# Kernel tuning notes

Hardware: AMD Instinct MI355X
Metric: run time of the kernel (lower is better)

## Reference

```python
import jax, jax.numpy as jnp
import numpy as np

ENC_HID = 512
DEC_HID = 1024
ATTN_DIM = 1024
ATTN_IN = ENC_HID * 2 + DEC_HID  # 2048
B, S = 32, 1024


def setup_inputs() -> dict:
    key = jax.random.key(0)
    k1, k2, k3, k4, k5 = jax.random.split(key, 5)
    decoder_hidden = jax.random.normal(k1, (B, DEC_HID), dtype=jnp.float32)
    encoder_outputs = jax.random.normal(k2, (B, S, 2 * ENC_HID), dtype=jnp.float32)
    # nn.Linear(attn_in, attn_dim): weight [attn_dim, attn_in], bias [attn_dim]
    lim = 1.0 / np.sqrt(ATTN_IN)
    W = jax.random.uniform(k3, (ATTN_IN, ATTN_DIM), jnp.float32, -lim, lim)
    b = jax.random.uniform(k4, (ATTN_DIM,), jnp.float32, -lim, lim)
    v = jax.random.uniform(k5, (ATTN_DIM,), jnp.float32, 0.0, 1.0)
    return {"decoder_hidden": decoder_hidden, "encoder_outputs": encoder_outputs,
            "W": W, "b": b, "v": v}


def reference(decoder_hidden, encoder_outputs, W, b, v):
    # Avoid materializing the repeat+concat: split the Linear weight into the
    # decoder-hidden block and the encoder-outputs block. Same math as
    # tanh(Linear(cat([dec_rep, enc], -1))).
    W_dec = W[:DEC_HID]          # [dec_hid, attn_dim]
    W_enc = W[DEC_HID:]          # [2*enc_hid, attn_dim]
    dec_proj = decoder_hidden @ W_dec + b                     # [B, A]
    enc_proj = jnp.einsum('bse,ea->bsa', encoder_outputs, W_enc)  # [B, S, A]
    energy = jnp.tanh(enc_proj + dec_proj[:, None, :])        # [B, S, A]
    attention = jnp.einsum('bsa,a->bs', energy, v)            # [B, S]
    return jax.nn.softmax(attention, axis=1)
```

## Files before the change

### kernel.cpp

```cpp
#include <hip/hip_runtime.h>
#include <stdint.h>

#define ENC2 1024
#define DECH 1024
#define ADIM 1024
#define BB   32
#define SS   1024

typedef _Float16 half_t;
typedef __attribute__((ext_vector_type(4))) _Float16 half4;
typedef __attribute__((ext_vector_type(8))) _Float16 half8;
typedef __attribute__((ext_vector_type(4))) float    f32x4;

__device__ __forceinline__ void dma16(const half_t* g, half_t* l) {
    __builtin_amdgcn_global_load_lds((const __attribute__((address_space(1))) void*)g,
                                     (__attribute__((address_space(3))) void*)l,
                                     16, 0, 0);
}

#define VM6()   asm volatile("s_waitcnt vmcnt(6)" ::: "memory")
#define VM3()   asm volatile("s_waitcnt vmcnt(3)" ::: "memory")
#define VM0()   asm volatile("s_waitcnt vmcnt(0)" ::: "memory")
#define LGKM0() asm volatile("s_waitcnt lgkmcnt(0)" ::: "memory")
#define SCHED0() __builtin_amdgcn_sched_barrier(0)
#define RBAR()  __builtin_amdgcn_s_barrier()

__global__ __launch_bounds__(512) void k_prep(const float* __restrict__ enc,
                                              const float* __restrict__ W,
                                              const float* __restrict__ dh,
                                              half_t* __restrict__ e16,
                                              half_t* __restrict__ Wt2,
                                              float* __restrict__ dpart) {
    __shared__ __align__(16) char smem[33792];
    const int bid = blockIdx.x;
    const int t = threadIdx.x;

    if (bid < 2048) {
        half_t (*Lt)[264] = (half_t (*)[264])smem;
        const int rblk = bid >> 2, cblk = bid & 3;
        const int r0 = rblk * 64, k0 = cblk * 256;
        #pragma unroll
        for (int i = 0; i < 8; i++) {
            int row = i * 8 + (t >> 6);
            int col = (t & 63) * 4;
            float4 vv = *(const float4*)&enc[(size_t)(r0 + row) * ENC2 + k0 + col];
            half4 h;
            h[0] = (half_t)vv.x; h[1] = (half_t)vv.y;
            h[2] = (half_t)vv.z; h[3] = (half_t)vv.w;
            *(half4*)&Lt[row][col] = h;
        }
        __syncthreads();
        const int mi = rblk >> 1, p = rblk & 1;
        const int ks0 = cblk * 8;
        #pragma unroll
        for (int j = 0; j < 4; j++) {
            int u = j * 512 + t;
            int pair = u >> 6, l = u & 63;
            int ksl = pair >> 2, quad = pair & 3;
            half8 h = *(const half8*)&Lt[l][ksl * 32 + quad * 8];
            size_t chunk = (size_t)(mi * 32 + ks0 + ksl) * 8 + quad * 2 + p;
            *(half8*)&e16[(chunk << 9) + l * 8] = h;
        }
    } else if (bid < 2176) {
        float (*tile)[257] = (float (*)[257])smem;
        const int blk = bid - 2048;
        const int nb = blk >> 5;
        const int ks = blk & 31;
        #pragma unroll
        for (int i = 0; i < 16; i++) {
            int idx = t + i * 512;
            int kr = idx >> 8, n = idx & 255;
            tile[kr][n] = W[(size_t)(DECH + ks * 32 + kr) * ADIM + nb * 256 + n];
        }
        __syncthreads();
        half_t* reg = Wt2 + ((size_t)(nb * 32 + ks) << 13);
        #pragma unroll
        for (int i = 0; i < 2; i++) {
            int cid = t + i * 512;
            int r = cid >> 2, pos = cid & 3;
            int c = pos ^ ((r >> 1) & 3);
            half8 h;
            #pragma unroll
            for (int e = 0; e < 8; e++) h[e] = (half_t)tile[c * 8 + e][r];
            *(half8*)(reg + r * 32 + pos * 8) = h;
        }
    } else {
        float (*red)[BB][64] = (float (*)[BB][64])smem;
        const int blk = bid - 2176;
        const int ct = blk & 15;
        const int kc = blk >> 4;
        if (t < 256) {
            const int col = ct * 64 + (t & 63);
            const int w = t >> 6;
            const int k0 = kc * 128 + w * 32;
            float wreg[32];
            #pragma unroll
            for (int kk = 0; kk < 32; kk++)
                wreg[kk] = W[(size_t)(k0 + kk) * ADIM + col];
            float s[BB];
            #pragma unroll
            for (int b = 0; b < BB; b++) s[b] = 0.f;
            #pragma unroll
            for (int kk = 0; kk < 32; kk++) {
                #pragma unroll
                for (int b = 0; b < BB; b++)
                    s[b] += dh[b * DECH + k0 + kk] * wreg[kk];
            }
            #pragma unroll
            for (int b = 0; b < BB; b++) red[w][b][t & 63] = s[b];
        }
        __syncthreads();
        if (t < 64) {
            for (int b = 0; b < BB; b++)
                dpart[((size_t)kc * BB + b) * ADIM + ct * 64 + t] =
                    red[0][b][t] + red[1][b][t] + red[2][b][t] + red[3][b][t];
        }
    }
}

#define BM 128
#define BN 256
#define BK 32

__global__ __launch_bounds__(512, 4) void k_main(const half_t* __restrict__ encA,
                                                 const half_t* __restrict__ Wt2,
                                                 const float* __restrict__ dpart,
                                                 const float* __restrict__ bias,
                                                 const float* __restrict__ v,
                                                 float* __restrict__ scores_part) {
    __shared__ half_t lsA[3][4096];
    __shared__ half_t lsB[3][8192];

    const int bid = blockIdx.x;
    const int mi = (bid >> 5) * 8 + (bid & 7);
    const int nb = (bid >> 3) & 3;
    const int m0 = mi * BM;
    const int t = threadIdx.x;
    const int w = t >> 6, L = t & 63;
    const int wm = w & 1, wn = w >> 1;
    const int lane15 = L & 15, quad = L >> 4;

    const half_t* Abase = encA + ((size_t)mi << 17);
    const half_t* Bbase = Wt2 + ((size_t)(nb * 32) << 13);

    f32x4 acc[4][4];
    #pragma unroll
    for (int i = 0; i < 4; i++)
        #pragma unroll
        for (int j = 0; j < 4; j++) acc[i][j] = (f32x4)0.f;

    auto stage = [&](int ks, int pb) {
        dma16(Abase + (((size_t)ks * 8 + w) << 9) + L * 8, &lsA[pb][w * 512]);
        #pragma unroll
        for (int jj = 0; jj < 2; jj++) {
            int j = 2 * w + jj;
            dma16(Bbase + ((size_t)ks << 13) + j * 512 + L * 8,
                  &lsB[pb][j * 512]);
        }
    };

    stage(0, 0);
    stage(1, 1);

    int cur = 0;
    for (int ks = 0; ks < ENC2 / BK; ks++) {
        const int nxt = (cur == 0) ? 2 : cur - 1;
        if (ks < ENC2 / BK - 2) {
            stage(ks + 2, nxt);
            VM6();
        } else if (ks == ENC2 / BK - 2) {
            VM3();
        } else {
            VM0();
        }
        RBAR();
        SCHED0();

        half8 af[4], bf[4];
        #pragma unroll
        for (int sm = 0; sm < 4; sm++)
            af[sm] = *(const half8*)&lsA[cur][quad * 1024 +
                                              (wm * 64 + sm * 16 + lane15) * 8];
        #pragma unroll
        for (int sn = 0; sn < 4; sn++) {
            int r = wn * 64 + sn * 16 + lane15;
            int pos = quad ^ ((r >> 1) & 3);
            bf[sn] = *(const half8*)&lsB[cur][r * 32 + pos * 8];
        }
        LGKM0();
        SCHED0();
        #pragma unroll
        for (int sm = 0; sm < 4; sm++)
            #pragma unroll
            for (int sn = 0; sn < 4; sn++)
                acc[sm][sn] = __builtin_amdgcn_mfma_f32_16x16x32_f16(
                    af[sm], bf[sn], acc[sm][sn], 0, 0, 0);
        RBAR();
        cur = (cur == 2) ? 0 : cur + 1;
    }

    const int batch = mi >> 3;
    float vv[4], dp[4];
    #pragma unroll
    for (int sn = 0; sn < 4; sn++) {
        int ng = nb * BN + wn * 64 + sn * 16 + lane15;
        vv[sn] = v[ng];
        float s = bias[ng];
        #pragma unroll
        for (int kc = 0; kc < 8; kc++)
            s += dpart[((size_t)kc * BB + batch) * ADIM + ng];
        dp[sn] = s;
    }

    float* redL = (float*)&lsA[0][0];
    #pragma unroll
    for (int sm = 0; sm < 4; sm++) {
        #pragma unroll
        for (int rr = 0; rr < 4; rr++) {
            float s = 0.f;
            #pragma unroll
            for (int sn = 0; sn < 4; sn++) {
                float x = acc[sm][sn][rr] + dp[sn];
                float e  = __builtin_amdgcn_exp2f(x * 2.8853900817779268f);
                float th = 1.f - 2.f * __builtin_amdgcn_rcpf(e + 1.f);
                s += th * vv[sn];
            }
            s += __shfl_xor(s, 1, 64);
            s += __shfl_xor(s, 2, 64);
            s += __shfl_xor(s, 4, 64);
            s += __shfl_xor(s, 8, 64);
            if (lane15 == 0) {
                int mlocal = wm * 64 + sm * 16 + quad * 4 + rr;
                redL[wn * 128 + mlocal] = s;
            }
        }
    }
    __syncthreads();
    if (t < 128) {
        float s = redL[t] + redL[128 + t] + redL[256 + t] + redL[384 + t];
        scores_part[((size_t)nb << 15) + m0 + t] = s;
    }
}

__global__ __launch_bounds__(256) void k_softmax(const float* __restrict__ sp,
                                                 float* __restrict__ out) {
    __shared__ float red[8];
    const int b = blockIdx.x, t = threadIdx.x;
    float x[4];
    #pragma unroll
    for (int i = 0; i < 4; i++) {
        size_t idx = (size_t)b * SS + t + i * 256;
        x[i] = sp[idx] + sp[(1u << 15) + idx] + sp[(2u << 15) + idx] +
               sp[(3u << 15) + idx];
    }
    float mx = fmaxf(fmaxf(x[0], x[1]), fmaxf(x[2], x[3]));
    #pragma unroll
    for (int d = 1; d < 64; d <<= 1) mx = fmaxf(mx, __shfl_xor(mx, d, 64));
    if ((t & 63) == 0) red[t >> 6] = mx;
    __syncthreads();
    mx = fmaxf(fmaxf(red[0], red[1]), fmaxf(red[2], red[3]));
    float e[4], s = 0.f;
    #pragma unroll
    for (int i = 0; i < 4; i++) {
        e[i] = __builtin_amdgcn_exp2f((x[i] - mx) * 1.4426950408889634f);
        s += e[i];
    }
    #pragma unroll
    for (int d = 1; d < 64; d <<= 1) s += __shfl_xor(s, d, 64);
    if ((t & 63) == 0) red[4 + (t >> 6)] = s;
    __syncthreads();
    s = red[4] + red[5] + red[6] + red[7];
    float inv = 1.f / s;
    #pragma unroll
    for (int i = 0; i < 4; i++) out[(size_t)b * SS + t + i * 256] = e[i] * inv;
}

__global__ __launch_bounds__(256) void k_wt_f(const float* __restrict__ W,
                                              half_t* __restrict__ Wt2) {
    __shared__ float tile[32][257];
    const int nb = blockIdx.x >> 5;
    const int ks = blockIdx.x & 31;
    const int t = threadIdx.x;
    #pragma unroll
    for (int i = 0; i < 32; i++) {
        int idx = t + i * 256;
        int kr = idx >> 8, n = idx & 255;
        tile[kr][n] = W[(size_t)(DECH + ks * 32 + kr) * ADIM + nb * 256 + n];
    }
    __syncthreads();
    half_t* reg = Wt2 + ((size_t)(nb * 32 + ks) << 13);
    #pragma unroll
    for (int i = 0; i < 4; i++) {
        int cid = t + i * 256;
        int r = cid >> 2, pos = cid & 3;
        int c = pos ^ ((r >> 1) & 3);
        half8 h;
        #pragma unroll
        for (int e = 0; e < 8; e++) h[e] = (half_t)tile[c * 8 + e][r];
        *(half8*)(reg + r * 32 + pos * 8) = h;
    }
}

__global__ __launch_bounds__(256) void k_dp1_f(const float* __restrict__ dh,
                                               const float* __restrict__ W,
                                               float* __restrict__ part) {
    __shared__ float red[4][BB][64];
    const int t = threadIdx.x;
    const int ct = blockIdx.x & 15;
    const int kc = blockIdx.x >> 4;
    const int col = ct * 64 + (t & 63);
    const int w = t >> 6;
    const int k0 = kc * 128 + w * 32;
    float wreg[32];
    #pragma unroll
    for (int kk = 0; kk < 32; kk++)
        wreg[kk] = W[(size_t)(k0 + kk) * ADIM + col];
    float s[BB];
    #pragma unroll
    for (int b = 0; b < BB; b++) s[b] = 0.f;
    #pragma unroll
    for (int kk = 0; kk < 32; kk++) {
        #pragma unroll
        for (int b = 0; b < BB; b++)
            s[b] += dh[b * DECH + k0 + kk] * wreg[kk];
    }
    #pragma unroll
    for (int b = 0; b < BB; b++) red[w][b][t & 63] = s[b];
    __syncthreads();
    if (t < 64) {
        for (int b = 0; b < BB; b++)
            part[((size_t)kc * BB + b) * ADIM + ct * 64 + t] =
                red[0][b][t] + red[1][b][t] + red[2][b][t] + red[3][b][t];
    }
}

__global__ __launch_bounds__(256) void k_dp2_f(const float* __restrict__ part,
                                               const float* __restrict__ bias,
                                               float* __restrict__ decp) {
    const int i = blockIdx.x * 256 + threadIdx.x;
    float s = bias[i & (ADIM - 1)];
    #pragma unroll
    for (int kc = 0; kc < 8; kc++)
        s += part[(size_t)kc * BB * ADIM + i];
    decp[i] = s;
}

#define LDA 40
__global__ __launch_bounds__(512, 4) void k_main_reg(const float* __restrict__ enc,
                                                     const half_t* __restrict__ Wt2,
                                                     const float* __restrict__ decp,
                                                     const float* __restrict__ v,
                                                     float* __restrict__ scores_part) {
    __shared__ half_t lsA[2][BM][LDA];
    __shared__ half_t lsB[2][BN * BK];

    const int bid = blockIdx.x;
    const int mi = (bid >> 5) * 8 + (bid & 7);
    const int nb = (bid >> 3) & 3;
    const int m0 = mi * BM;
    const int t = threadIdx.x;
    const int w = t >> 6, L = t & 63;
    const int wm = w & 1, wn = w >> 1;
    const int lane15 = L & 15, quad = L >> 4;

    const int arow = t & 127;
    const int akc  = (t >> 7) * 8;
    const float* Aptr = enc + (size_t)(m0 + arow) * ENC2 + akc;
    const half_t* Bbase = Wt2 + ((size_t)(nb * 32) << 13);

    f32x4 acc[4][4];
    #pragma unroll
    for (int i = 0; i < 4; i++)
        #pragma unroll
        for (int j = 0; j < 4; j++) acc[i][j] = (f32x4)0.f;

    float4 ra0, ra1;
    auto loadA = [&](int ks) {
        const float* p = Aptr + ks * BK;
        ra0 = *(const float4*)p;
        ra1 = *(const float4*)(p + 4);
    };
    auto writeA = [&](int pb) {
        half8 ha;
        ha[0] = (half_t)ra0.x; ha[1] = (half_t)ra0.y;
        ha[2] = (half_t)ra0.z; ha[3] = (half_t)ra0.w;
        ha[4] = (half_t)ra1.x; ha[5] = (half_t)ra1.y;
        ha[6] = (half_t)ra1.z; ha[7] = (half_t)ra1.w;
        *(half8*)&lsA[pb][arow][akc] = ha;
    };
    auto dmaB = [&](int ks, int pb) {
        #pragma unroll
        for (int jj = 0; jj < 2; jj++) {
            int j = 2 * w + jj;
            dma16(Bbase + ((size_t)ks << 13) + j * 512 + L * 8,
                  &lsB[pb][j * 512]);
        }
    };

    dmaB(0, 0);
    loadA(0);
    writeA(0);
    loadA(1);
    __syncthreads();

    for (int ks = 0; ks < ENC2 / BK; ks++) {
        const int cur = ks & 1;
        if (ks < ENC2 / BK - 1) {
            dmaB(ks + 1, cur ^ 1);
            writeA(cur ^ 1);
            if (ks < ENC2 / BK - 2) loadA(ks + 2);
        }
        half8 af[4], bf[4];
        #pragma unroll
        for (int sm = 0; sm < 4; sm++)
            af[sm] = *(const half8*)&lsA[cur][wm * 64 + sm * 16 + lane15][quad * 8];
        #pragma unroll
        for (int sn = 0; sn < 4; sn++) {
            int r = wn * 64 + sn * 16 + lane15;
            int pos = quad ^ ((r >> 1) & 3);
            bf[sn] = *(const half8*)&lsB[cur][r * 32 + pos * 8];
        }
        #pragma unroll
        for (int sm = 0; sm < 4; sm++)
            #pragma unroll
            for (int sn = 0; sn < 4; sn++)
                acc[sm][sn] = __builtin_amdgcn_mfma_f32_16x16x32_f16(
                    af[sm], bf[sn], acc[sm][sn], 0, 0, 0);
        __syncthreads();
    }

    const int batch = mi >> 3;
    float vv[4], dp[4];
    #pragma unroll
    for (int sn = 0; sn < 4; sn++) {
        int ng = nb * BN + wn * 64 + sn * 16 + lane15;
        vv[sn] = v[ng];
        dp[sn] = decp[(size_t)batch * ADIM + ng];
    }

    float* redL = (float*)&lsA[0][0][0];
    #pragma unroll
    for (int sm = 0; sm < 4; sm++) {
        #pragma unroll
        for (int rr = 0; rr < 4; rr++) {
            float s = 0.f;
            #pragma unroll
            for (int sn = 0; sn < 4; sn++) {
                float x = acc[sm][sn][rr] + dp[sn];
                float e  = __builtin_amdgcn_exp2f(x * 2.8853900817779268f);
                float th = 1.f - 2.f * __builtin_amdgcn_rcpf(e + 1.f);
                s += th * vv[sn];
            }
            s += __shfl_xor(s, 1, 64);
            s += __shfl_xor(s, 2, 64);
            s += __shfl_xor(s, 4, 64);
            s += __shfl_xor(s, 8, 64);
            if (lane15 == 0) {
                int mlocal = wm * 64 + sm * 16 + quad * 4 + rr;
                redL[wn * 128 + mlocal] = s;
            }
        }
    }
    __syncthreads();
    if (t < 128) {
        float s = redL[t] + redL[128 + t] + redL[256 + t] + redL[384 + t];
        scores_part[((size_t)nb << 15) + m0 + t] = s;
    }
}

extern "C" void kernel_launch(void* const* d_in, const int* in_sizes, int n_in,
                              void* d_out, int out_size, void* d_ws, size_t ws_size,
                              hipStream_t stream) {
    const float* dh   = (const float*)d_in[0];
    const float* enc  = (const float*)d_in[1];
    const float* W    = (const float*)d_in[2];
    const float* bias = (const float*)d_in[3];
    const float* v    = (const float*)d_in[4];
    float* out = (float*)d_out;

    char* ws = (char*)d_ws;
    const size_t E16_BYTES = (size_t)BB * SS * ENC2 * sizeof(half_t);
    const size_t NEED = (4u << 20) + E16_BYTES;

    if (ws_size >= NEED) {
        half_t* Wt2   = (half_t*)ws;
        float*  dpart = (float*)(ws + (2u << 20));
        float*  spart = (float*)(ws + (3u << 20));
        half_t* e16   = (half_t*)(ws + (4u << 20));

        k_prep   <<<2304, 512, 0, stream>>>(enc, W, dh, e16, Wt2, dpart);
        k_main   <<<1024, 512, 0, stream>>>(e16, Wt2, dpart, bias, v, spart);
        k_softmax<<<32, 256, 0, stream>>>(spart, out);
    } else {
        half_t* Wt2   = (half_t*)ws;
        float*  decp  = (float*)(ws + 2u * 1024 * 1024);
        float*  spart = (float*)(ws + 2u * 1024 * 1024 + 128 * 1024);
        float*  dpart = (float*)(ws + 2u * 1024 * 1024 + 640 * 1024);

        k_wt_f   <<<128, 256, 0, stream>>>(W, Wt2);
        k_dp1_f  <<<128, 256, 0, stream>>>(dh, W, dpart);
        k_dp2_f  <<<128, 256, 0, stream>>>(dpart, bias, decp);
        k_main_reg<<<1024, 512, 0, stream>>>(enc, Wt2, decp, v, spart);
        k_softmax<<<32, 256, 0, stream>>>(spart, out);
    }
}
```

Before: 281.3 us.

## Store fp16 encoder in row-major order and gather tiles directly in GEMM DMA

The prep kernel no longer reorders the fp16 encoder copy into a tiled chunk layout through shared memory. It now does a straight elementwise fp32-to-fp16 conversion in row-major order. The GEMM's global-to-LDS DMA addresses are changed to pull each lane's 16-byte piece from the row-major matrix at stride 1024. This drops the LDS transpose and its barrier from the prep pass, but the GEMM's A loads become strided per lane instead of contiguous 1 KB chunks, which may reduce coalescing.

```diff
diff --git a/kernel.cpp b/kernel.cpp
--- a/kernel.cpp
+++ b/kernel.cpp
@@ -36,30 +36,18 @@
     const int t = threadIdx.x;
 
     if (bid < 2048) {
-        half_t (*Lt)[264] = (half_t (*)[264])smem;
-        const int rblk = bid >> 2, cblk = bid & 3;
-        const int r0 = rblk * 64, k0 = cblk * 256;
-        #pragma unroll
-        for (int i = 0; i < 8; i++) {
-            int row = i * 8 + (t >> 6);
-            int col = (t & 63) * 4;
-            float4 vv = *(const float4*)&enc[(size_t)(r0 + row) * ENC2 + k0 + col];
-            half4 h;
-            h[0] = (half_t)vv.x; h[1] = (half_t)vv.y;
-            h[2] = (half_t)vv.z; h[3] = (half_t)vv.w;
-            *(half4*)&Lt[row][col] = h;
-        }
-        __syncthreads();
-        const int mi = rblk >> 1, p = rblk & 1;
-        const int ks0 = cblk * 8;
-        #pragma unroll
-        for (int j = 0; j < 4; j++) {
-            int u = j * 512 + t;
-            int pair = u >> 6, l = u & 63;
-            int ksl = pair >> 2, quad = pair & 3;
-            half8 h = *(const half8*)&Lt[l][ksl * 32 + quad * 8];
-            size_t chunk = (size_t)(mi * 32 + ks0 + ksl) * 8 + quad * 2 + p;
-            *(half8*)&e16[(chunk << 9) + l * 8] = h;
+        const size_t base = (size_t)bid * 16384 + t * 8;
+        #pragma unroll
+        for (int it = 0; it < 4; it++) {
+            size_t i = base + (size_t)it * 4096;
+            float4 a = *(const float4*)&enc[i];
+            float4 b = *(const float4*)&enc[i + 4];
+            half8 h;
+            h[0] = (half_t)a.x; h[1] = (half_t)a.y;
+            h[2] = (half_t)a.z; h[3] = (half_t)a.w;
+            h[4] = (half_t)b.x; h[5] = (half_t)b.y;
+            h[6] = (half_t)b.z; h[7] = (half_t)b.w;
+            *(half8*)&e16[i] = h;
         }
     } else if (bid < 2176) {
         float (*tile)[257] = (float (*)[257])smem;
@@ -143,6 +131,8 @@
     const half_t* Abase = encA + ((size_t)mi << 17);
     const half_t* Bbase = Wt2 + ((size_t)(nb * 32) << 13);
 
+    const size_t aoff = ((size_t)((w & 1) * 64 + L)) * 1024 + ((w >> 1) << 3);
+
     f32x4 acc[4][4];
     #pragma unroll
     for (int i = 0; i < 4; i++)
@@ -150,7 +140,7 @@
         for (int j = 0; j < 4; j++) acc[i][j] = (f32x4)0.f;
 
     auto stage = [&](int ks, int pb) {
-        dma16(Abase + (((size_t)ks * 8 + w) << 9) + L * 8, &lsA[pb][w * 512]);
+        dma16(Abase + aoff + ks * 32, &lsA[pb][w * 512]);
         #pragma unroll
         for (int jj = 0; jj < 2; jj++) {
             int j = 2 * w + jj;
```

Result: slower. 302.2 us (+7.4%).
